# Optimization experiments

Measured on AMD Instinct MI355X. Metric: run time of the kernel, lower is better.

The kernel has to match this reference:

```python
import jax, jax.numpy as jnp
import numpy as np

N_NODES = 100000
N_EDGES = 1600000
N_GRAPHS = 512
HIDDEN = 64
HEADS = 4
HEAD_DIM = HIDDEN // HEADS
IN_FEAT = 32
EDGE_FEAT = 16
N_CLASSES = 10
N_CONV = 3
BN_EPS = 1e-5
BN_BIAS = 1e-4  # torch init: weight=1, bias=0.0001
NEG_SLOPE = 0.2


def batchnorm(x):
    # training-mode BatchNorm1d with weight=1, bias=1e-4 (biased variance, as torch)
    mu = jnp.mean(x, axis=0)
    var = jnp.var(x, axis=0)
    return (x - mu) * jax.lax.rsqrt(var + BN_EPS) + BN_BIAS


def segment_softmax(logits, seg, num_segments):
    # logits: [E] or [E,H]; softmax over edges sharing the same seg id (dst node)
    m = jax.ops.segment_max(logits, seg, num_segments=num_segments)
    e = jnp.exp(logits - m[seg])
    s = jax.ops.segment_sum(e, seg, num_segments=num_segments)
    return e / s[seg]


def setup_inputs() -> dict:
    key = jax.random.key(0)
    ks = jax.random.split(key, 24)
    sd = 0.1
    inp = {}
    inp["x"] = jax.random.normal(ks[0], (N_NODES, IN_FEAT), dtype=jnp.float32)
    inp["edge_attr"] = jax.random.normal(ks[1], (N_EDGES, EDGE_FEAT), dtype=jnp.float32)
    inp["edge_index"] = jax.random.randint(ks[2], (2, N_EDGES), 0, N_NODES)
    inp["batch"] = jnp.sort(jax.random.randint(ks[3], (N_NODES,), 0, N_GRAPHS))
    # EGAT (conv_feat): node/edge linear maps + attention vector
    inp["egat_Wx"] = jax.random.normal(ks[4], (IN_FEAT, HIDDEN), dtype=jnp.float32) * sd
    inp["egat_bx"] = jnp.zeros((HIDDEN,), dtype=jnp.float32)
    inp["egat_We"] = jax.random.normal(ks[5], (EDGE_FEAT, HIDDEN), dtype=jnp.float32) * sd
    inp["egat_be"] = jnp.zeros((HIDDEN,), dtype=jnp.float32)
    inp["egat_att"] = jax.random.normal(ks[6], (HIDDEN,), dtype=jnp.float32) * sd
    # 3 stacked GATConv layers (PyG-style, edge_dim=hidden, concat heads)
    inp["conv_W"] = jax.random.normal(ks[7], (N_CONV, HIDDEN, HIDDEN), dtype=jnp.float32) * sd
    inp["conv_We"] = jax.random.normal(ks[8], (N_CONV, HIDDEN, HIDDEN), dtype=jnp.float32) * sd
    inp["conv_att_src"] = jax.random.normal(ks[9], (N_CONV, HEADS, HEAD_DIM), dtype=jnp.float32) * sd
    inp["conv_att_dst"] = jax.random.normal(ks[10], (N_CONV, HEADS, HEAD_DIM), dtype=jnp.float32) * sd
    inp["conv_att_edge"] = jax.random.normal(ks[11], (N_CONV, HEADS, HEAD_DIM), dtype=jnp.float32) * sd
    inp["conv_bias"] = jnp.zeros((N_CONV, HIDDEN), dtype=jnp.float32)
    # FC head: one hidden Linear (num_fc_layers=2) + classifier
    inp["lin_W"] = jax.random.normal(ks[12], (HIDDEN, HIDDEN), dtype=jnp.float32) * sd
    inp["lin_b"] = jnp.zeros((HIDDEN,), dtype=jnp.float32)
    inp["cls_W"] = jax.random.normal(ks[13], (HIDDEN, N_CLASSES), dtype=jnp.float32) * sd
    inp["cls_b"] = jnp.zeros((N_CLASSES,), dtype=jnp.float32)
    return inp


def reference(x, edge_attr, edge_index, batch,
              egat_Wx, egat_bx, egat_We, egat_be, egat_att,
              conv_W, conv_We, conv_att_src, conv_att_dst, conv_att_edge, conv_bias,
              lin_W, lin_b, cls_W, cls_b):
    src, dst = edge_index[0], edge_index[1]
    n = x.shape[0]

    x = batchnorm(x)

    # EGAT: gather -> attend (leaky_relu + segment softmax over dst) -> scatter-add
    h = x @ egat_Wx + egat_bx            # [N, hidden]
    he = edge_attr @ egat_We + egat_be   # [E, hidden]
    s = jax.nn.leaky_relu((h[src] + h[dst] + he) @ egat_att, NEG_SLOPE)  # [E]
    alpha = segment_softmax(s, dst, n)
    x = jax.ops.segment_sum(alpha[:, None] * h[src], dst, num_segments=n)
    edge = he
    x = jax.nn.relu(x)
    edge = jax.nn.relu(edge)

    # stacked GATConv layers (multi-head, edge features modulate attention)
    for i in range(N_CONV):
        xb = batchnorm(x)
        hh = (xb @ conv_W[i]).reshape(n, HEADS, HEAD_DIM)            # [N,H,D]
        ee = (edge @ conv_We[i]).reshape(-1, HEADS, HEAD_DIM)        # [E,H,D]
        a = (jnp.sum(hh[src] * conv_att_src[i], -1)
             + jnp.sum(hh[dst] * conv_att_dst[i], -1)
             + jnp.sum(ee * conv_att_edge[i], -1))                   # [E,H]
        a = jax.nn.leaky_relu(a, NEG_SLOPE)
        a = segment_softmax(a, dst, n)
        out = jax.ops.segment_sum(a[..., None] * hh[src], dst, num_segments=n)
        x = jax.nn.relu(out.reshape(n, HIDDEN) + conv_bias[i])

    # global add pool over graphs
    x = jax.ops.segment_sum(x, batch, num_segments=N_GRAPHS)  # [G, hidden]

    x = batchnorm(x)
    x = jax.nn.relu(x @ lin_W + lin_b)
    x = batchnorm(x)
    # dropout disabled (eval-mode determinism)
    x = x @ cls_W + cls_b
    return jax.nn.log_softmax(x, axis=-1)
```

## Files before the change

kernel.cpp:

```cpp
#include <hip/hip_runtime.h>
#include <math.h>

#define NN 100000
#define NE 1600000
#define NG 512
#define NCLS 10
#define NEG 0.2f
#define BNEPS 1e-5f
#define BNB 1e-4f
#define MNEG -1e30f

#define NBUK 391
#define CHUNK2 6144
#define NB2 261
#define CAP3 5120

typedef unsigned short u16;
typedef unsigned int u32;
typedef _Float16 f16;
typedef __attribute__((ext_vector_type(8))) f16 f16x8;
typedef __attribute__((ext_vector_type(4))) float f32x4;

__device__ __forceinline__ float lrelu(float v) { return v > 0.f ? v : NEG * v; }
__device__ __forceinline__ u16 f2h(float x) { union { u16 s; f16 h; } c; c.h = (f16)x; return c.s; }
__device__ __forceinline__ float h2f(u16 s) { union { u16 s; f16 h; } c; c.s = s; return (float)c.h; }

template<int C>
__global__ __launch_bounds__(256) void k_bn_part(const float* __restrict__ x, int rows,
                                                 float* __restrict__ part) {
    const int RPI = 256 / C;
    int col = threadIdx.x % C;
    int sub = threadIdx.x / C;
    int nb = gridDim.x;
    int rpb = (rows + nb - 1) / nb;
    int r0 = blockIdx.x * rpb;
    int r1 = min(rows, r0 + rpb);
    float s = 0.f, q = 0.f;
    for (int r = r0 + sub; r < r1; r += RPI) {
        float v = x[(size_t)r * C + col];
        s += v; q += v * v;
    }
    __shared__ float ls[256], lq[256];
    ls[threadIdx.x] = s; lq[threadIdx.x] = q;
    __syncthreads();
    for (int st = RPI / 2; st > 0; st >>= 1) {
        if (sub < st) {
            ls[threadIdx.x] += ls[threadIdx.x + st * C];
            lq[threadIdx.x] += lq[threadIdx.x + st * C];
        }
        __syncthreads();
    }
    if (sub == 0) {
        part[(size_t)blockIdx.x * C + col] = ls[col];
        part[(size_t)(nb + blockIdx.x) * C + col] = lq[col];
    }
}

__global__ __launch_bounds__(256) void k_bn_part16(const u16* __restrict__ x, int rows,
                                                   float* __restrict__ part) {
    int col = threadIdx.x & 63;
    int sub = threadIdx.x >> 6;
    int nb = gridDim.x;
    int rpb = (rows + nb - 1) / nb;
    int r0 = blockIdx.x * rpb;
    int r1 = min(rows, r0 + rpb);
    float s = 0.f, q = 0.f;
    for (int r = r0 + sub; r < r1; r += 4) {
        float v = h2f(x[(size_t)r * 64 + col]);
        s += v; q += v * v;
    }
    __shared__ float ls[256], lq[256];
    ls[threadIdx.x] = s; lq[threadIdx.x] = q;
    __syncthreads();
    for (int st = 2; st > 0; st >>= 1) {
        if (sub < st) {
            ls[threadIdx.x] += ls[threadIdx.x + st * 64];
            lq[threadIdx.x] += lq[threadIdx.x + st * 64];
        }
        __syncthreads();
    }
    if (sub == 0) {
        part[(size_t)blockIdx.x * 64 + col] = ls[col];
        part[(size_t)(nb + blockIdx.x) * 64 + col] = lq[col];
    }
}

__global__ __launch_bounds__(64) void k_bn_adj(const float* __restrict__ part, int nb, int rows, int C,
                                               const float* __restrict__ W, const float* __restrict__ b,
                                               int Ncol, float* __restrict__ sc, float* __restrict__ badj) {
    int c = threadIdx.x;
    __shared__ float shl[64];
    if (c < C) {
        float s = 0.f, q = 0.f;
        for (int bb = 0; bb < nb; bb++) {
            s += part[(size_t)bb * C + c];
            q += part[(size_t)(nb + bb) * C + c];
        }
        float mu = s / rows;
        float var = q / rows - mu * mu;
        float sl = rsqrtf(var + BNEPS);
        sc[c] = sl;
        shl[c] = BNB - mu * sl;
    }
    __syncthreads();
    if (c < Ncol) {
        float a = b ? b[c] : 0.f;
        for (int k = 0; k < C; k++) a += shl[k] * W[(size_t)k * Ncol + c];
        badj[c] = a;
    }
}

template<int C>
__global__ __launch_bounds__(256) void k_bnadjf(const float* __restrict__ part, int nb, int rows,
                                                const float* __restrict__ W, const float* __restrict__ b,
                                                float* __restrict__ badj, u16* __restrict__ Bff) {
    int t = threadIdx.x;
    int c = t & 63, seg = t >> 6;
    __shared__ float rs[4][64], rq[4][64];
    __shared__ float scl[64], shl[64];
    float s = 0.f, q = 0.f;
    if (c < C)
        for (int bb = seg; bb < nb; bb += 4) {
            s += part[(size_t)bb * C + c];
            q += part[(size_t)(nb + bb) * C + c];
        }
    rs[seg][c] = s; rq[seg][c] = q;
    __syncthreads();
    if (t < C) {
        float ss = rs[0][t] + rs[1][t] + rs[2][t] + rs[3][t];
        float qq = rq[0][t] + rq[1][t] + rq[2][t] + rq[3][t];
        float mu = ss / rows;
        float var = qq / rows - mu * mu;
        float sl = rsqrtf(var + BNEPS);
        scl[t] = sl; shl[t] = BNB - mu * sl;
    }
    __syncthreads();
    float a = 0.f;
    for (int k = seg; k < C; k += 4) a += shl[k] * W[(size_t)k * 64 + c];
    rs[seg][c] = a;
    __syncthreads();
    if (t < 64) badj[t] = (b ? b[t] : 0.f) + rs[0][t] + rs[1][t] + rs[2][t] + rs[3][t];
    const int KB = C / 32;
    for (int idx = t; idx < 4 * KB * 64 * 8; idx += 256) {
        int j = idx & 7;
        int lane = (idx >> 3) & 63;
        int kb = (idx >> 9) % KB;
        int ct = idx / (KB * 512);
        int k = kb * 32 + (lane >> 4) * 8 + j;
        int col = ct * 16 + (lane & 15);
        Bff[idx] = f2h(scl[k] * W[(size_t)k * 64 + col]);
    }
}

template<int KB, int EPI, bool F32IN>
__global__ __launch_bounds__(256) void k_gemm_mf(const void* __restrict__ xin,
                                                 const u16* __restrict__ Bff,
                                                 const float* __restrict__ badj,
                                                 u16* __restrict__ outb, int rows,
                                                 const float* __restrict__ att, float* __restrict__ hs,
                                                 const float* __restrict__ as_, const float* __restrict__ ad_,
                                                 float* __restrict__ asrc, float* __restrict__ adst) {
    int wid = threadIdx.x >> 6, lane = threadIdx.x & 63;
    int er = lane & 15, kh = lane >> 4;
    int r0 = blockIdx.x * 64;
    int rw = r0 + wid * 16;
    __shared__ u16 Dl[64][68];
    f16x8 bf[4][KB];
#pragma unroll
    for (int ct = 0; ct < 4; ct++)
#pragma unroll
        for (int kb = 0; kb < KB; kb++)
            bf[ct][kb] = *(const f16x8*)(Bff + ((size_t)(ct * KB + kb) * 64 + lane) * 8);
    f16x8 af[KB];
    int arow = rw + er;
    if (F32IN) {
        const float* xf = (const float*)xin;
        f16x8 av = (f16x8)(f16)0.f;
        if (arow < rows) {
            const float4* p = (const float4*)(xf + (size_t)arow * 32 + kh * 8);
            float4 v0 = p[0], v1 = p[1];
            av[0] = (f16)v0.x; av[1] = (f16)v0.y; av[2] = (f16)v0.z; av[3] = (f16)v0.w;
            av[4] = (f16)v1.x; av[5] = (f16)v1.y; av[6] = (f16)v1.z; av[7] = (f16)v1.w;
        }
        af[0] = av;
    } else {
        const u16* xh = (const u16*)xin;
#pragma unroll
        for (int kb = 0; kb < KB; kb++) {
            f16x8 av = (f16x8)(f16)0.f;
            if (arow < rows) av = *(const f16x8*)(xh + (size_t)arow * 64 + kb * 32 + kh * 8);
            af[kb] = av;
        }
    }
    f32x4 d[4];
#pragma unroll
    for (int ct = 0; ct < 4; ct++) {
        float bj = badj[ct * 16 + er];
        f32x4 cc = {bj, bj, bj, bj};
#pragma unroll
        for (int kb = 0; kb < KB; kb++)
            cc = __builtin_amdgcn_mfma_f32_16x16x32_f16(af[kb], bf[ct][kb], cc, 0, 0, 0);
        d[ct] = cc;
    }
#pragma unroll
    for (int ct = 0; ct < 4; ct++)
#pragma unroll
        for (int r = 0; r < 4; r++)
            Dl[wid * 16 + kh * 4 + r][ct * 16 + er] = f2h(d[ct][r]);
    if (EPI == 1) {
        float av[4];
#pragma unroll
        for (int ct = 0; ct < 4; ct++) av[ct] = att[ct * 16 + er];
#pragma unroll
        for (int r = 0; r < 4; r++) {
            float v = d[0][r] * av[0] + d[1][r] * av[1] + d[2][r] * av[2] + d[3][r] * av[3];
#pragma unroll
            for (int o = 1; o < 16; o <<= 1) v += __shfl_xor(v, o);
            int rr = rw + kh * 4 + r;
            if (er == 0 && rr < rows) hs[rr] = v;
        }
    }
    if (EPI == 2) {
        float a1v[4], a2v[4];
#pragma unroll
        for (int ct = 0; ct < 4; ct++) { a1v[ct] = as_[ct * 16 + er]; a2v[ct] = ad_[ct * 16 + er]; }
#pragma unroll
        for (int ct = 0; ct < 4; ct++) {
#pragma unroll
            for (int r = 0; r < 4; r++) {
                float s1 = d[ct][r] * a1v[ct], s2 = d[ct][r] * a2v[ct];
#pragma unroll
                for (int o = 1; o < 16; o <<= 1) { s1 += __shfl_xor(s1, o); s2 += __shfl_xor(s2, o); }
                int rr = rw + kh * 4 + r;
                if (er == 0 && rr < rows) {
                    asrc[(size_t)rr * 4 + ct] = s1;
                    adst[(size_t)rr * 4 + ct] = s2;
                }
            }
        }
    }
    __syncthreads();
    const u32* D32 = (const u32*)&Dl[0][0];
    u32* out32 = (u32*)outb;
    for (int idx = threadIdx.x; idx < 64 * 32; idx += 256) {
        int r = idx >> 5, c2 = idx & 31;
        int rr = r0 + r;
        if (rr < rows) out32[(size_t)rr * 32 + c2] = D32[r * 34 + c2];
    }
}

__global__ __launch_bounds__(256) void k_gemm_head(const float* __restrict__ x, const float* __restrict__ W,
                                                   const float* __restrict__ sc, const float* __restrict__ badj,
                                                   float* __restrict__ outf, int rows) {
    __shared__ float Ws[64 * 64];
    __shared__ float Xs[32 * 64];
    int r0 = blockIdx.x * 32;
    for (int i = threadIdx.x; i < 64 * 64; i += 256) Ws[i] = W[i];
    for (int i = threadIdx.x; i < 32 * 64; i += 256) {
        int r = i / 64, k = i % 64;
        int rr = r0 + r;
        Xs[i] = (rr < rows) ? x[(size_t)rr * 64 + k] * sc[k] : 0.f;
    }
    __syncthreads();
    int col = threadIdx.x & 63;
    int rg = threadIdx.x >> 6;
    float b0 = badj[col];
    float acc[8];
#pragma unroll
    for (int i = 0; i < 8; i++) acc[i] = b0;
    for (int k = 0; k < 64; k++) {
        float w = Ws[k * 64 + col];
#pragma unroll
        for (int i = 0; i < 8; i++) acc[i] += Xs[(rg * 8 + i) * 64 + k] * w;
    }
#pragma unroll
    for (int i = 0; i < 8; i++) {
        int r = r0 + rg * 8 + i;
        if (r < rows) outf[(size_t)r * 64 + col] = fmaxf(acc[i], 0.f);
    }
}

__global__ __launch_bounds__(768) void k_we(const float* __restrict__ cWe, const float* __restrict__ cae,
                                            const float* __restrict__ Wee, const float* __restrict__ att,
                                            const float* __restrict__ bee, float* __restrict__ wEbuf,
                                            u16* __restrict__ Bf1, u16* __restrict__ Bf2) {
    int t = threadIdx.x;
    int l = t >> 8;
    int h = (t >> 6) & 3;
    int k = t & 63;
    float a = 0.f;
    for (int d = 0; d < 16; d++)
        a += cWe[(size_t)l * 4096 + k * 64 + h * 16 + d] * cae[l * 64 + h * 16 + d];
    wEbuf[t] = a;
    if (t < 16) {
        float v = 0.f;
        for (int j = 0; j < 64; j++) v += Wee[t * 64 + j] * att[j];
        wEbuf[768 + t] = v;
    }
    if (t == 16) {
        float v = 0.f;
        for (int j = 0; j < 64; j++) v += bee[j] * att[j];
        wEbuf[784] = v;
    }
    for (int idx = t; idx < 4 * 64 * 8; idx += 768) {
        int cb = idx >> 9, ln = (idx >> 3) & 63, j = idx & 7;
        int col = cb * 16 + (ln & 15);
        int kk = (ln >> 4) * 8 + j;
        float v = (kk < 16) ? Wee[kk * 64 + col] : 0.f;
        Bf1[idx] = f2h(v);
    }
    __syncthreads();
    for (int idx = t; idx < 2 * 64 * 8; idx += 768) {
        int kb = idx >> 9, ln = (idx >> 3) & 63, j = idx & 7;
        int n = ln & 15;
        int kk = kb * 32 + (ln >> 4) * 8 + j;
        float v = (n < 12) ? wEbuf[n * 64 + kk] : 0.f;
        Bf2[idx] = f2h(v);
    }
}

__global__ __launch_bounds__(256) void k_bhist(const int* __restrict__ dst, int* __restrict__ hist) {
    __shared__ int lh[512];
    int t = threadIdx.x;
    lh[t] = 0; lh[t + 256] = 0;
    __syncthreads();
    int base = blockIdx.x * CHUNK2;
    int cnt = min(CHUNK2, NE - base);
    for (int i = t; i < cnt; i += 256) atomicAdd(&lh[dst[base + i] >> 8], 1);
    __syncthreads();
    for (int b = t; b < NBUK; b += 256) hist[blockIdx.x * NBUK + b] = lh[b];
}

__global__ __launch_bounds__(256) void k_colsum(const int* __restrict__ hist, int* __restrict__ colsum) {
    int col = blockIdx.x;
    int t = threadIdx.x;
    int s = 0;
    for (int b = t; b < NB2; b += 256) s += hist[b * NBUK + col];
    __shared__ int ls[256];
    ls[t] = s;
    __syncthreads();
    for (int st = 128; st; st >>= 1) {
        if (t < st) ls[t] += ls[t + st];
        __syncthreads();
    }
    if (t == 0) colsum[col] = ls[0];
}

__global__ __launch_bounds__(512) void k_bukscan(const int* __restrict__ colsum,
                                                 int* __restrict__ bucketBase, int* __restrict__ rowp) {
    __shared__ int ls[512];
    int t = threadIdx.x;
    int v = (t < NBUK) ? colsum[t] : 0;
    ls[t] = v;
    __syncthreads();
    for (int off = 1; off < 512; off <<= 1) {
        int a = (t >= off) ? ls[t - off] : 0;
        __syncthreads();
        ls[t] += a;
        __syncthreads();
    }
    if (t < NBUK) bucketBase[t] = ls[t] - v;
    if (t == 0) { bucketBase[NBUK] = NE; rowp[NN] = NE; }
}

__global__ __launch_bounds__(512) void k_coloffs(const int* __restrict__ hist,
                                                 const int* __restrict__ bucketBase, int* __restrict__ offs) {
    int col = blockIdx.x;
    int t = threadIdx.x;
    __shared__ int ls[512];
    int v = (t < NB2) ? hist[(size_t)t * NBUK + col] : 0;
    ls[t] = v;
    __syncthreads();
    for (int off = 1; off < 512; off <<= 1) {
        int a = (t >= off) ? ls[t - off] : 0;
        __syncthreads();
        ls[t] += a;
        __syncthreads();
    }
    if (t < NB2) offs[(size_t)t * NBUK + col] = bucketBase[col] + ls[t] - v;
}

__global__ __launch_bounds__(256) void k_part(const int* __restrict__ src, const int* __restrict__ dst,
                                              const int* __restrict__ offs, int2* __restrict__ seTmp) {
    __shared__ int lhist[512];
    __shared__ int lstart[NBUK + 1];
    __shared__ int lcur[NBUK];
    __shared__ int loffs[NBUK];
    __shared__ int2 stage[CHUNK2];
    int t = threadIdx.x;
    int base = blockIdx.x * CHUNK2;
    int cnt = min(CHUNK2, NE - base);
    int blkrow = blockIdx.x * NBUK;
    lhist[t] = 0; lhist[t + 256] = 0;
    __syncthreads();
    for (int i = t; i < cnt; i += 256) atomicAdd(&lhist[dst[base + i] >> 8], 1);
    __syncthreads();
    for (int off = 1; off < 512; off <<= 1) {
        int v0 = (t >= off) ? lhist[t - off] : 0;
        int v1 = lhist[t + 256 - off];
        __syncthreads();
        lhist[t] += v0; lhist[t + 256] += v1;
        __syncthreads();
    }
    if (t == 0) lstart[0] = 0;
    lstart[t + 1] = lhist[t];
    if (t + 257 <= NBUK) lstart[t + 257] = lhist[t + 256];
    __syncthreads();
    for (int b = t; b < NBUK; b += 256) {
        lcur[b] = lstart[b];
        loffs[b] = offs[blkrow + b];
    }
    __syncthreads();
    for (int i = t; i < cnt; i += 256) {
        int e = base + i;
        int d = dst[e];
        int b = d >> 8;
        int pos = atomicAdd(&lcur[b], 1);
        int2 v; v.x = src[e] | (b << 17); v.y = e | ((d & 255) << 21);
        stage[pos] = v;
    }
    __syncthreads();
    for (int q = t; q < cnt; q += 256) {
        int2 v = stage[q];
        int b = ((u32)v.x) >> 17;
        int2 o; o.x = v.x & 0x1FFFF; o.y = v.y;
        seTmp[loffs[b] + (q - lstart[b])] = o;
    }
}

__global__ __launch_bounds__(256) void k_bucket(const int2* __restrict__ seTmp,
                                                const int* __restrict__ bucketBase,
                                                int2* __restrict__ se, int* __restrict__ rowp) {
    int b = blockIdx.x;
    int t = threadIdx.x;
    int beg = bucketBase[b], end = bucketBase[b + 1];
    int cnt = end - beg;
    __shared__ int lhist[256], lscan[256], lcur[256];
    __shared__ int2 ebuf[CAP3];
    lhist[t] = 0;
    __syncthreads();
    for (int i = t; i < cnt; i += 256)
        atomicAdd(&lhist[((u32)seTmp[beg + i].y) >> 21], 1);
    __syncthreads();
    lscan[t] = lhist[t];
    __syncthreads();
    for (int off = 1; off < 256; off <<= 1) {
        int v = (t >= off) ? lscan[t - off] : 0;
        __syncthreads();
        lscan[t] += v;
        __syncthreads();
    }
    int excl = lscan[t] - lhist[t];
    lcur[t] = excl;
    int node = b * 256 + t;
    if (node < NN) rowp[node] = beg + excl;
    __syncthreads();
    if (cnt <= CAP3) {
        for (int i = t; i < cnt; i += 256) {
            int2 v = seTmp[beg + i];
            int dl = ((u32)v.y) >> 21;
            int pos = atomicAdd(&lcur[dl], 1);
            int2 o; o.x = v.x; o.y = v.y & 0x1FFFFF;
            ebuf[pos] = o;
        }
        __syncthreads();
        for (int q = t; q < cnt; q += 256) se[beg + q] = ebuf[q];
    } else {
        for (int i = t; i < cnt; i += 256) {
            int2 v = seTmp[beg + i];
            int dl = ((u32)v.y) >> 21;
            int pos = atomicAdd(&lcur[dl], 1);
            int2 o; o.x = v.x; o.y = v.y & 0x1FFFFF;
            se[beg + pos] = o;
        }
    }
}

__global__ __launch_bounds__(256) void k_edgepre(const float* __restrict__ ea,
                                                 const u16* __restrict__ Bf1, const u16* __restrict__ Bf2,
                                                 const float* __restrict__ bee, const float* __restrict__ wEbuf,
                                                 const int2* __restrict__ se,
                                                 float* __restrict__ heatt, ushort4* __restrict__ aedH) {
    int wid = threadIdx.x >> 6, lane = threadIdx.x & 63;
    int gw = blockIdx.x * 4 + wid;
    int p0 = gw * 16;
    __shared__ f16 Pl[4][16][72];
    __shared__ f16 D2l[4][16][20];
    f16x8 bf1[4], bf2[2];
#pragma unroll
    for (int cb = 0; cb < 4; cb++) bf1[cb] = *(const f16x8*)(Bf1 + ((size_t)cb * 64 + lane) * 8);
#pragma unroll
    for (int kb = 0; kb < 2; kb++) bf2[kb] = *(const f16x8*)(Bf2 + ((size_t)kb * 64 + lane) * 8);
    int er = lane & 15, kh = lane >> 4;
    f16x8 af = (f16x8)(f16)0.f;
    float part = 0.f;
    if (kh < 2) {
        int e = se[p0 + er].y;
        const float4* pa = (const float4*)(ea + (size_t)e * 16 + kh * 8);
        float4 v0 = pa[0], v1 = pa[1];
        af[0] = (f16)v0.x; af[1] = (f16)v0.y; af[2] = (f16)v0.z; af[3] = (f16)v0.w;
        af[4] = (f16)v1.x; af[5] = (f16)v1.y; af[6] = (f16)v1.z; af[7] = (f16)v1.w;
        const float* va = wEbuf + 768 + kh * 8;
        part = v0.x * va[0] + v0.y * va[1] + v0.z * va[2] + v0.w * va[3]
             + v1.x * va[4] + v1.y * va[5] + v1.z * va[6] + v1.w * va[7];
    }
    float po = __shfl_xor(part, 16);
    if (lane < 16) heatt[p0 + lane] = part + po + wEbuf[784];
    f32x4 z = {0.f, 0.f, 0.f, 0.f};
    f32x4 d0 = __builtin_amdgcn_mfma_f32_16x16x32_f16(af, bf1[0], z, 0, 0, 0);
    f32x4 d1 = __builtin_amdgcn_mfma_f32_16x16x32_f16(af, bf1[1], z, 0, 0, 0);
    f32x4 d2_ = __builtin_amdgcn_mfma_f32_16x16x32_f16(af, bf1[2], z, 0, 0, 0);
    f32x4 d3 = __builtin_amdgcn_mfma_f32_16x16x32_f16(af, bf1[3], z, 0, 0, 0);
    {
        float b0 = bee[0 * 16 + er], b1 = bee[1 * 16 + er], b2 = bee[2 * 16 + er], b3 = bee[3 * 16 + er];
#pragma unroll
        for (int r = 0; r < 4; r++) {
            int row = kh * 4 + r;
            Pl[wid][row][0 * 16 + er] = (f16)fmaxf(d0[r] + b0, 0.f);
            Pl[wid][row][1 * 16 + er] = (f16)fmaxf(d1[r] + b1, 0.f);
            Pl[wid][row][2 * 16 + er] = (f16)fmaxf(d2_[r] + b2, 0.f);
            Pl[wid][row][3 * 16 + er] = (f16)fmaxf(d3[r] + b3, 0.f);
        }
    }
    __syncthreads();
    f16x8 pa0 = *(const f16x8*)&Pl[wid][er][kh * 8];
    f16x8 pa1 = *(const f16x8*)&Pl[wid][er][32 + kh * 8];
    f32x4 dd = __builtin_amdgcn_mfma_f32_16x16x32_f16(pa0, bf2[0], z, 0, 0, 0);
    dd = __builtin_amdgcn_mfma_f32_16x16x32_f16(pa1, bf2[1], dd, 0, 0, 0);
#pragma unroll
    for (int r = 0; r < 4; r++) D2l[wid][kh * 4 + r][er] = (f16)dd[r];
    __syncthreads();
    int e2 = lane & 15, l3 = lane >> 4;
    if (l3 < 3) {
        ushort4 o = *(const ushort4*)&D2l[wid][e2][l3 * 4];
        aedH[(size_t)l3 * NE + p0 + e2] = o;
    }
}

__global__ __launch_bounds__(256) void k_egat_agg(const int* __restrict__ rowp, const int2* __restrict__ se,
                                                  const float* __restrict__ heatt, const float* __restrict__ hs,
                                                  const u16* __restrict__ hb, u16* __restrict__ xout) {
    int wid = threadIdx.x >> 6, lane = threadIdx.x & 63;
    int n = blockIdx.x * 4 + wid;
    if (n >= NN) return;
    int beg = rowp[n], deg = rowp[n + 1] - beg;
    if (deg == 0) { xout[(size_t)n * 64 + lane] = 0; return; }
    float hsn = hs[n];
    int half = lane >> 5;
    int c0 = (lane & 31) * 2;
    if (deg <= 64) {
        int s = 0; float lg = MNEG;
        if (lane < deg) {
            int2 pr = se[beg + lane];
            s = pr.x;
            lg = lrelu(hs[s] + hsn + heatt[beg + lane]);
        }
        float m = lg;
#pragma unroll
        for (int o = 32; o; o >>= 1) m = fmaxf(m, __shfl_xor(m, o));
        float e = (lane < deg) ? __expf(lg - m) : 0.f;
        float sm = e;
#pragma unroll
        for (int o = 32; o; o >>= 1) sm += __shfl_xor(sm, o);
        float p = e * (1.f / sm);
        float a0 = 0.f, a1 = 0.f, a2 = 0.f, a3 = 0.f;
        for (int j = 0; j < deg; j += 4) {
            int j0 = j + half, j1 = j + 2 + half;
            int s0 = __shfl(s, j0); float p0 = __shfl(p, j0);
            int s1 = __shfl(s, j1); float p1 = __shfl(p, j1);
            u32 v0 = *(const u32*)(hb + (size_t)s0 * 64 + c0);
            u32 v1 = *(const u32*)(hb + (size_t)s1 * 64 + c0);
            a0 = fmaf(p0, h2f((u16)v0), a0);
            a1 = fmaf(p0, h2f((u16)(v0 >> 16)), a1);
            a2 = fmaf(p1, h2f((u16)v1), a2);
            a3 = fmaf(p1, h2f((u16)(v1 >> 16)), a3);
        }
        a0 += a2; a1 += a3;
        a0 += __shfl_xor(a0, 32);
        a1 += __shfl_xor(a1, 32);
        if (lane < 32) {
            u32 o = (u32)f2h(fmaxf(a0, 0.f)) | ((u32)f2h(fmaxf(a1, 0.f)) << 16);
            ((u32*)xout)[(size_t)n * 32 + (lane & 31)] = o;
        }
    } else {
        float m = MNEG, sm = 0.f;
        for (int i = lane; i < deg; i += 64) {
            int2 pr = se[beg + i];
            float v = lrelu(hs[pr.x] + hsn + heatt[beg + i]);
            float mn = fmaxf(m, v);
            sm = sm * __expf(m - mn) + __expf(v - mn);
            m = mn;
        }
#pragma unroll
        for (int o = 32; o; o >>= 1) {
            float mo = __shfl_xor(m, o), so = __shfl_xor(sm, o);
            float mn = fmaxf(m, mo);
            sm = sm * __expf(m - mn) + so * __expf(mo - mn);
            m = mn;
        }
        float inv = 1.f / sm;
        float acc0 = 0.f;
        for (int base = 0; base < deg; base += 64) {
            int i = base + lane;
            int s = 0; float p = 0.f;
            if (i < deg) {
                int2 pr = se[beg + i];
                s = pr.x;
                p = __expf(lrelu(hs[s] + hsn + heatt[beg + i]) - m) * inv;
            }
            int mm = min(64, deg - base);
            for (int j = 0; j < mm; j++) {
                int s0 = __shfl(s, j); float q0 = __shfl(p, j);
                acc0 = fmaf(q0, h2f(hb[(size_t)s0 * 64 + lane]), acc0);
            }
        }
        xout[(size_t)n * 64 + lane] = f2h(fmaxf(acc0, 0.f));
    }
}

__global__ __launch_bounds__(256) void k_conv_agg(const int* __restrict__ rowp, const int2* __restrict__ se,
                                                  const ushort4* __restrict__ aedH, const float* __restrict__ asrc,
                                                  const float* __restrict__ adst, const u16* __restrict__ hb,
                                                  const float* __restrict__ bias, u16* __restrict__ xout) {
    int wid = threadIdx.x >> 6, lane = threadIdx.x & 63;
    int n = blockIdx.x * 4 + wid;
    if (n >= NN) return;
    int beg = rowp[n], deg = rowp[n + 1] - beg;
    if (deg == 0) { xout[(size_t)n * 64 + lane] = f2h(fmaxf(bias[lane], 0.f)); return; }
    float4 an = ((const float4*)adst)[n];
    __shared__ float pls[4][4][72];
    __shared__ int sl[4][64];
    int half = lane >> 5;
    int c0 = (lane & 31) * 2;
    if (deg <= 64) {
        int s = 0;
        float l0 = MNEG, l1 = MNEG, l2 = MNEG, l3 = MNEG;
        if (lane < deg) {
            s = se[beg + lane].x;
            float4 as4 = ((const float4*)asrc)[s];
            ushort4 u = aedH[beg + lane];
            l0 = lrelu(as4.x + an.x + h2f(u.x));
            l1 = lrelu(as4.y + an.y + h2f(u.y));
            l2 = lrelu(as4.z + an.z + h2f(u.z));
            l3 = lrelu(as4.w + an.w + h2f(u.w));
        }
        float m0 = l0, m1 = l1, m2 = l2, m3 = l3;
#pragma unroll
        for (int o = 32; o; o >>= 1) {
            m0 = fmaxf(m0, __shfl_xor(m0, o)); m1 = fmaxf(m1, __shfl_xor(m1, o));
            m2 = fmaxf(m2, __shfl_xor(m2, o)); m3 = fmaxf(m3, __shfl_xor(m3, o));
        }
        float e0 = (lane < deg) ? __expf(l0 - m0) : 0.f;
        float e1 = (lane < deg) ? __expf(l1 - m1) : 0.f;
        float e2 = (lane < deg) ? __expf(l2 - m2) : 0.f;
        float e3 = (lane < deg) ? __expf(l3 - m3) : 0.f;
        float s0 = e0, s1 = e1, s2 = e2, s3 = e3;
#pragma unroll
        for (int o = 32; o; o >>= 1) {
            s0 += __shfl_xor(s0, o); s1 += __shfl_xor(s1, o);
            s2 += __shfl_xor(s2, o); s3 += __shfl_xor(s3, o);
        }
        pls[wid][0][lane] = e0 * (1.f / s0);
        pls[wid][1][lane] = e1 * (1.f / s1);
        pls[wid][2][lane] = e2 * (1.f / s2);
        pls[wid][3][lane] = e3 * (1.f / s3);
        sl[wid][lane] = s;
        __builtin_amdgcn_wave_barrier();
        int head = (lane & 31) >> 3;
        const float* prow = &pls[wid][head][0];
        const int* srow = &sl[wid][0];
        float a0 = 0.f, a1 = 0.f, a2 = 0.f, a3 = 0.f;
        for (int j = 0; j < deg; j += 4) {
            int j0 = j + half, j1 = j + 2 + half;
            float p0 = prow[j0]; int sj0 = srow[j0];
            float p1 = prow[j1]; int sj1 = srow[j1];
            u32 v0 = *(const u32*)(hb + (size_t)sj0 * 64 + c0);
            u32 v1 = *(const u32*)(hb + (size_t)sj1 * 64 + c0);
            a0 = fmaf(p0, h2f((u16)v0), a0);
            a1 = fmaf(p0, h2f((u16)(v0 >> 16)), a1);
            a2 = fmaf(p1, h2f((u16)v1), a2);
            a3 = fmaf(p1, h2f((u16)(v1 >> 16)), a3);
        }
        a0 += a2; a1 += a3;
        a0 += __shfl_xor(a0, 32);
        a1 += __shfl_xor(a1, 32);
        if (lane < 32) {
            u32 o = (u32)f2h(fmaxf(a0 + bias[c0], 0.f)) | ((u32)f2h(fmaxf(a1 + bias[c0 + 1], 0.f)) << 16);
            ((u32*)xout)[(size_t)n * 32 + (lane & 31)] = o;
        }
    } else {
        int hq = lane >> 4;
        float m0 = MNEG, m1 = MNEG, m2 = MNEG, m3 = MNEG;
        float s0 = 0.f, s1 = 0.f, s2 = 0.f, s3 = 0.f;
        for (int i = lane; i < deg; i += 64) {
            int s = se[beg + i].x;
            float4 as4 = ((const float4*)asrc)[s];
            ushort4 u = aedH[beg + i];
            float l0 = lrelu(as4.x + an.x + h2f(u.x));
            float l1 = lrelu(as4.y + an.y + h2f(u.y));
            float l2 = lrelu(as4.z + an.z + h2f(u.z));
            float l3 = lrelu(as4.w + an.w + h2f(u.w));
            float n0 = fmaxf(m0, l0); s0 = s0 * __expf(m0 - n0) + __expf(l0 - n0); m0 = n0;
            float n1 = fmaxf(m1, l1); s1 = s1 * __expf(m1 - n1) + __expf(l1 - n1); m1 = n1;
            float n2 = fmaxf(m2, l2); s2 = s2 * __expf(m2 - n2) + __expf(l2 - n2); m2 = n2;
            float n3 = fmaxf(m3, l3); s3 = s3 * __expf(m3 - n3) + __expf(l3 - n3); m3 = n3;
        }
#pragma unroll
        for (int o = 32; o; o >>= 1) {
            float mo, so, mn;
            mo = __shfl_xor(m0, o); so = __shfl_xor(s0, o); mn = fmaxf(m0, mo);
            s0 = s0 * __expf(m0 - mn) + so * __expf(mo - mn); m0 = mn;
            mo = __shfl_xor(m1, o); so = __shfl_xor(s1, o); mn = fmaxf(m1, mo);
            s1 = s1 * __expf(m1 - mn) + so * __expf(mo - mn); m1 = mn;
            mo = __shfl_xor(m2, o); so = __shfl_xor(s2, o); mn = fmaxf(m2, mo);
            s2 = s2 * __expf(m2 - mn) + so * __expf(mo - mn); m2 = mn;
            mo = __shfl_xor(m3, o); so = __shfl_xor(s3, o); mn = fmaxf(m3, mo);
            s3 = s3 * __expf(m3 - mn) + so * __expf(mo - mn); m3 = mn;
        }
        float i0 = 1.f / s0, i1 = 1.f / s1, i2 = 1.f / s2, i3 = 1.f / s3;
        float acc0 = 0.f;
        for (int base = 0; base < deg; base += 64) {
            int i = base + lane;
            if (i < deg) {
                int s = se[beg + i].x;
                float4 as4 = ((const float4*)asrc)[s];
                ushort4 u = aedH[beg + i];
                pls[wid][0][lane] = __expf(lrelu(as4.x + an.x + h2f(u.x)) - m0) * i0;
                pls[wid][1][lane] = __expf(lrelu(as4.y + an.y + h2f(u.y)) - m1) * i1;
                pls[wid][2][lane] = __expf(lrelu(as4.z + an.z + h2f(u.z)) - m2) * i2;
                pls[wid][3][lane] = __expf(lrelu(as4.w + an.w + h2f(u.w)) - m3) * i3;
                sl[wid][lane] = s;
            }
            __builtin_amdgcn_wave_barrier();
            int mm = min(64, deg - base);
            const float* prow = &pls[wid][hq][0];
            const int* srow = &sl[wid][0];
            for (int j = 0; j < mm; j++)
                acc0 = fmaf(prow[j], h2f(hb[(size_t)srow[j] * 64 + lane]), acc0);
            __builtin_amdgcn_wave_barrier();
        }
        xout[(size_t)n * 64 + lane] = f2h(fmaxf(acc0 + bias[lane], 0.f));
    }
}

__device__ __forceinline__ int lowerb(const int* a, int n, int key) {
    int lo = 0, hi = n;
    while (lo < hi) {
        int mid = (lo + hi) >> 1;
        if (a[mid] < key) lo = mid + 1; else hi = mid;
    }
    return lo;
}

__global__ __launch_bounds__(256) void k_pool(const u16* __restrict__ x, const int* __restrict__ batch,
                                              float* __restrict__ g) {
    int gr = blockIdx.x;
    int lane = threadIdx.x & 63;
    int sub = threadIdx.x >> 6;
    int beg = lowerb(batch, NN, gr);
    int end = lowerb(batch, NN, gr + 1);
    float acc = 0.f;
    for (int i = beg + sub; i < end; i += 4) acc += h2f(x[(size_t)i * 64 + lane]);
    __shared__ float ls[4][64];
    ls[sub][lane] = acc;
    __syncthreads();
    if (sub == 0)
        g[(size_t)gr * 64 + lane] = ls[0][lane] + ls[1][lane] + ls[2][lane] + ls[3][lane];
}

__global__ __launch_bounds__(64) void k_cls(const float* __restrict__ y, const float* __restrict__ W,
                                            const float* __restrict__ sc, const float* __restrict__ badj,
                                            float* __restrict__ out) {
    int r = blockIdx.x, lane = threadIdx.x;
    __shared__ float yr[64];
    yr[lane] = y[(size_t)r * 64 + lane] * sc[lane];
    __syncthreads();
    float lg = -INFINITY;
    if (lane < NCLS) {
        float a = badj[lane];
        for (int k = 0; k < 64; k++) a += yr[k] * W[k * NCLS + lane];
        lg = a;
    }
    float mx = lg;
#pragma unroll
    for (int o = 32; o; o >>= 1) mx = fmaxf(mx, __shfl_xor(mx, o));
    float e = (lane < NCLS) ? expf(lg - mx) : 0.f;
    float s = e;
#pragma unroll
    for (int o = 32; o; o >>= 1) s += __shfl_xor(s, o);
    if (lane < NCLS) out[(size_t)r * NCLS + lane] = lg - mx - logf(s);
}

extern "C" void kernel_launch(void* const* d_in, const int* in_sizes, int n_in,
                              void* d_out, int out_size, void* d_ws, size_t ws_size,
                              hipStream_t stream) {
    const float* x0  = (const float*)d_in[0];
    const float* ea  = (const float*)d_in[1];
    const int* eidx  = (const int*)d_in[2];
    const int* batch = (const int*)d_in[3];
    const float* Wx  = (const float*)d_in[4];
    const float* bx  = (const float*)d_in[5];
    const float* Wee = (const float*)d_in[6];
    const float* bee = (const float*)d_in[7];
    const float* att = (const float*)d_in[8];
    const float* cW  = (const float*)d_in[9];
    const float* cWe = (const float*)d_in[10];
    const float* cas = (const float*)d_in[11];
    const float* cad = (const float*)d_in[12];
    const float* cae = (const float*)d_in[13];
    const float* cb  = (const float*)d_in[14];
    const float* lW  = (const float*)d_in[15];
    const float* lb  = (const float*)d_in[16];
    const float* clW = (const float*)d_in[17];
    const float* clb = (const float*)d_in[18];
    float* out = (float*)d_out;

    const int* srcA = eidx;
    const int* dstA = eidx + NE;

    char* w = (char*)d_ws;
    size_t off = 0;
    auto alloc = [&](size_t bytes) -> void* {
        void* p = w + off;
        off += (bytes + 255) & ~(size_t)255;
        return p;
    };
    u16* hbA      = (u16*)alloc((size_t)NN * 64 * 2);
    u16* B16      = (u16*)alloc((size_t)NN * 64 * 2);
    float* hs     = (float*)alloc((size_t)NN * 4);
    float* asrc   = (float*)alloc((size_t)NN * 4 * 4);
    float* adst   = (float*)alloc((size_t)NN * 4 * 4);
    float* heatt  = (float*)alloc((size_t)NE * 4);
    ushort4* aedH = (ushort4*)alloc((size_t)3 * NE * 8);
    int2* se      = (int2*)alloc((size_t)NE * 8);
    int* rowp     = (int*)alloc((size_t)(NN + 1) * 4);
    int* hist     = (int*)alloc((size_t)NB2 * NBUK * 4);
    int* offs     = (int*)alloc((size_t)NB2 * NBUK * 4);
    int* bucketBase = (int*)alloc((size_t)(NBUK + 1) * 4);
    int* colsum   = (int*)alloc((size_t)NBUK * 4);
    float* part   = (float*)alloc((size_t)2 * 200 * 64 * 4);
    float* badj   = (float*)alloc(64 * 4);
    float* wEbuf  = (float*)alloc(800 * 4);
    u16* Bf1      = (u16*)alloc(4 * 64 * 8 * 2);
    u16* Bf2      = (u16*)alloc(2 * 64 * 8 * 2);
    u16* Bff      = (u16*)alloc(8 * 64 * 8 * 2);
    float* g      = (float*)alloc((size_t)NG * 64 * 4);
    float* y      = (float*)alloc((size_t)NG * 64 * 4);
    float* badj2  = (float*)alloc(64 * 4);
    float* badj3  = (float*)alloc(64 * 4);
    float* sc2    = (float*)alloc(64 * 4);
    float* sc3    = (float*)alloc(64 * 4);
    if (off > ws_size) return;

    int2* seTmp = (int2*)aedH;

    const int NB = 200;
    const int GEMMB = (NN + 63) / 64;

    k_bhist<<<NB2, 256, 0, stream>>>(dstA, hist);
    k_colsum<<<NBUK, 256, 0, stream>>>(hist, colsum);
    k_bukscan<<<1, 512, 0, stream>>>(colsum, bucketBase, rowp);
    k_coloffs<<<NBUK, 512, 0, stream>>>(hist, bucketBase, offs);
    k_part<<<NB2, 256, 0, stream>>>(srcA, dstA, offs, seTmp);
    k_bucket<<<NBUK, 256, 0, stream>>>(seTmp, bucketBase, se, rowp);

    k_we<<<1, 768, 0, stream>>>(cWe, cae, Wee, att, bee, wEbuf, Bf1, Bf2);

    k_bn_part<32><<<NB, 256, 0, stream>>>(x0, NN, part);
    k_bnadjf<32><<<1, 256, 0, stream>>>(part, NB, NN, Wx, bx, badj, Bff);
    k_gemm_mf<1, 1, true><<<GEMMB, 256, 0, stream>>>(
        x0, Bff, badj, hbA, NN, att, hs, nullptr, nullptr, nullptr, nullptr);

    k_edgepre<<<NE / 64, 256, 0, stream>>>(ea, Bf1, Bf2, bee, wEbuf, se, heatt, aedH);

    k_egat_agg<<<(NN + 3) / 4, 256, 0, stream>>>(rowp, se, heatt, hs, hbA, B16);

    for (int l = 0; l < 3; l++) {
        k_bn_part16<<<NB, 256, 0, stream>>>(B16, NN, part);
        k_bnadjf<64><<<1, 256, 0, stream>>>(part, NB, NN, cW + (size_t)l * 4096, nullptr, badj, Bff);
        k_gemm_mf<2, 2, false><<<GEMMB, 256, 0, stream>>>(
            B16, Bff, badj, hbA, NN, nullptr, nullptr,
            cas + l * 64, cad + l * 64, asrc, adst);
        k_conv_agg<<<(NN + 3) / 4, 256, 0, stream>>>(rowp, se, aedH + (size_t)l * NE, asrc, adst, hbA,
                                                     cb + l * 64, B16);
    }

    k_pool<<<NG, 256, 0, stream>>>(B16, batch, g);

    k_bn_part<64><<<2, 256, 0, stream>>>(g, NG, part);
    k_bn_adj<<<1, 64, 0, stream>>>(part, 2, NG, 64, lW, lb, 64, sc2, badj2);
    k_gemm_head<<<(NG + 31) / 32, 256, 0, stream>>>(g, lW, sc2, badj2, y, NG);

    k_bn_part<64><<<2, 256, 0, stream>>>(y, NG, part);
    k_bn_adj<<<1, 64, 0, stream>>>(part, 2, NG, 64, clW, clb, 10, sc3, badj3);
    k_cls<<<NG, 64, 0, stream>>>(y, clW, sc3, badj3, out);
}
```

Baseline: 707.9 us.

## Process 32 edges per wave in edgepre and unroll aggregation gathers by 8

The edge precompute kernel now handles 32 edges per wave instead of 16. All 64 lanes load edge attributes into shared memory, and block-wide __syncthreads is replaced by wave barriers, which halves the grid and amortizes the weight-fragment loads. The EGAT and conv aggregation loops are unrolled to issue four independent neighbor gathers per iteration with more accumulators, giving more memory-level parallelism. Costs are higher register and LDS use, and relying on wave barriers assumes the shared-memory accesses stay within one wave. The unrolled loop reads up to 8 past deg, which relies on padding or masked probabilities being zero.

```diff
diff --git a/kernel.cpp b/kernel.cpp
--- a/kernel.cpp
+++ b/kernel.cpp
@@ -482,58 +482,80 @@
                                                  const int2* __restrict__ se,
                                                  float* __restrict__ heatt, ushort4* __restrict__ aedH) {
     int wid = threadIdx.x >> 6, lane = threadIdx.x & 63;
-    int gw = blockIdx.x * 4 + wid;
-    int p0 = gw * 16;
-    __shared__ f16 Pl[4][16][72];
-    __shared__ f16 D2l[4][16][20];
+    int p0 = (blockIdx.x * 4 + wid) * 32;
+    __shared__ f16 EaD[4][32][24];
+    __shared__ f16 Pl[4][32][72];
     f16x8 bf1[4], bf2[2];
 #pragma unroll
     for (int cb = 0; cb < 4; cb++) bf1[cb] = *(const f16x8*)(Bf1 + ((size_t)cb * 64 + lane) * 8);
 #pragma unroll
     for (int kb = 0; kb < 2; kb++) bf2[kb] = *(const f16x8*)(Bf2 + ((size_t)kb * 64 + lane) * 8);
+    int e = lane & 31, q = lane >> 5;
+    int ei = se[p0 + e].y;
+    const float4* pa = (const float4*)(ea + (size_t)ei * 16 + q * 8);
+    float4 v0 = pa[0], v1 = pa[1];
+    {
+        const float* va = wEbuf + 768 + q * 8;
+        float part = v0.x * va[0] + v0.y * va[1] + v0.z * va[2] + v0.w * va[3]
+                   + v1.x * va[4] + v1.y * va[5] + v1.z * va[6] + v1.w * va[7];
+        float po = __shfl_xor(part, 32);
+        if (lane < 32) heatt[p0 + e] = part + po + wEbuf[784];
+    }
+    {
+        f16x8 t;
+        t[0] = (f16)v0.x; t[1] = (f16)v0.y; t[2] = (f16)v0.z; t[3] = (f16)v0.w;
+        t[4] = (f16)v1.x; t[5] = (f16)v1.y; t[6] = (f16)v1.z; t[7] = (f16)v1.w;
+        *(f16x8*)&EaD[wid][e][q * 8] = t;
+    }
+    __builtin_amdgcn_wave_barrier();
     int er = lane & 15, kh = lane >> 4;
-    f16x8 af = (f16x8)(f16)0.f;
-    float part = 0.f;
+    f16x8 a0f = (f16x8)(f16)0.f, a1f = (f16x8)(f16)0.f;
     if (kh < 2) {
-        int e = se[p0 + er].y;
-        const float4* pa = (const float4*)(ea + (size_t)e * 16 + kh * 8);
-        float4 v0 = pa[0], v1 = pa[1];
-        af[0] = (f16)v0.x; af[1] = (f16)v0.y; af[2] = (f16)v0.z; af[3] = (f16)v0.w;
-        af[4] = (f16)v1.x; af[5] = (f16)v1.y; af[6] = (f16)v1.z; af[7] = (f16)v1.w;
-        const float* va = wEbuf + 768 + kh * 8;
-        part = v0.x * va[0] + v0.y * va[1] + v0.z * va[2] + v0.w * va[3]
-             + v1.x * va[4] + v1.y * va[5] + v1.z * va[6] + v1.w * va[7];
-    }
-    float po = __shfl_xor(part, 16);
-    if (lane < 16) heatt[p0 + lane] = part + po + wEbuf[784];
+        a0f = *(const f16x8*)&EaD[wid][er][kh * 8];
+        a1f = *(const f16x8*)&EaD[wid][16 + er][kh * 8];
+    }
     f32x4 z = {0.f, 0.f, 0.f, 0.f};
-    f32x4 d0 = __builtin_amdgcn_mfma_f32_16x16x32_f16(af, bf1[0], z, 0, 0, 0);
-    f32x4 d1 = __builtin_amdgcn_mfma_f32_16x16x32_f16(af, bf1[1], z, 0, 0, 0);
-    f32x4 d2_ = __builtin_amdgcn_mfma_f32_16x16x32_f16(af, bf1[2], z, 0, 0, 0);
-    f32x4 d3 = __builtin_amdgcn_mfma_f32_16x16x32_f16(af, bf1[3], z, 0, 0, 0);
+    f32x4 d0[4], d1[4];
+#pragma unroll
+    for (int ct = 0; ct < 4; ct++) {
+        d0[ct] = __builtin_amdgcn_mfma_f32_16x16x32_f16(a0f, bf1[ct], z, 0, 0, 0);
+        d1[ct] = __builtin_amdgcn_mfma_f32_16x16x32_f16(a1f, bf1[ct], z, 0, 0, 0);
+    }
     {
-        float b0 = bee[0 * 16 + er], b1 = bee[1 * 16 + er], b2 = bee[2 * 16 + er], b3 = bee[3 * 16 + er];
-#pragma unroll
-        for (int r = 0; r < 4; r++) {
-            int row = kh * 4 + r;
-            Pl[wid][row][0 * 16 + er] = (f16)fmaxf(d0[r] + b0, 0.f);
-            Pl[wid][row][1 * 16 + er] = (f16)fmaxf(d1[r] + b1, 0.f);
-            Pl[wid][row][2 * 16 + er] = (f16)fmaxf(d2_[r] + b2, 0.f);
-            Pl[wid][row][3 * 16 + er] = (f16)fmaxf(d3[r] + b3, 0.f);
-        }
-    }
-    __syncthreads();
-    f16x8 pa0 = *(const f16x8*)&Pl[wid][er][kh * 8];
-    f16x8 pa1 = *(const f16x8*)&Pl[wid][er][32 + kh * 8];
-    f32x4 dd = __builtin_amdgcn_mfma_f32_16x16x32_f16(pa0, bf2[0], z, 0, 0, 0);
-    dd = __builtin_amdgcn_mfma_f32_16x16x32_f16(pa1, bf2[1], dd, 0, 0, 0);
-#pragma unroll
-    for (int r = 0; r < 4; r++) D2l[wid][kh * 4 + r][er] = (f16)dd[r];
-    __syncthreads();
-    int e2 = lane & 15, l3 = lane >> 4;
-    if (l3 < 3) {
-        ushort4 o = *(const ushort4*)&D2l[wid][e2][l3 * 4];
+#pragma unroll
+        for (int ct = 0; ct < 4; ct++) {
+            float bb = bee[ct * 16 + er];
+#pragma unroll
+            for (int r = 0; r < 4; r++) {
+                Pl[wid][kh * 4 + r][ct * 16 + er] = (f16)fmaxf(d0[ct][r] + bb, 0.f);
+                Pl[wid][16 + kh * 4 + r][ct * 16 + er] = (f16)fmaxf(d1[ct][r] + bb, 0.f);
+            }
+        }
+    }
+    __builtin_amdgcn_wave_barrier();
+    f16x8 pa00 = *(const f16x8*)&Pl[wid][er][kh * 8];
+    f16x8 pa01 = *(const f16x8*)&Pl[wid][er][32 + kh * 8];
+    f16x8 pa10 = *(const f16x8*)&Pl[wid][16 + er][kh * 8];
+    f16x8 pa11 = *(const f16x8*)&Pl[wid][16 + er][32 + kh * 8];
+    f32x4 dd0 = __builtin_amdgcn_mfma_f32_16x16x32_f16(pa00, bf2[0], z, 0, 0, 0);
+    dd0 = __builtin_amdgcn_mfma_f32_16x16x32_f16(pa01, bf2[1], dd0, 0, 0, 0);
+    f32x4 dd1 = __builtin_amdgcn_mfma_f32_16x16x32_f16(pa10, bf2[0], z, 0, 0, 0);
+    dd1 = __builtin_amdgcn_mfma_f32_16x16x32_f16(pa11, bf2[1], dd1, 0, 0, 0);
+    __builtin_amdgcn_wave_barrier();
+#pragma unroll
+    for (int r = 0; r < 4; r++) {
+        EaD[wid][kh * 4 + r][er] = (f16)dd0[r];
+        EaD[wid][16 + kh * 4 + r][er] = (f16)dd1[r];
+    }
+    __builtin_amdgcn_wave_barrier();
+    {
+        int e2 = lane & 31, l3 = lane >> 5;
+        ushort4 o = *(const ushort4*)&EaD[wid][e2][l3 * 4];
         aedH[(size_t)l3 * NE + p0 + e2] = o;
+        if (lane < 32) {
+            ushort4 o2 = *(const ushort4*)&EaD[wid][lane][8];
+            aedH[(size_t)2 * NE + p0 + lane] = o2;
+        }
     }
 }
 
@@ -564,18 +586,26 @@
         for (int o = 32; o; o >>= 1) sm += __shfl_xor(sm, o);
         float p = e * (1.f / sm);
         float a0 = 0.f, a1 = 0.f, a2 = 0.f, a3 = 0.f;
-        for (int j = 0; j < deg; j += 4) {
-            int j0 = j + half, j1 = j + 2 + half;
-            int s0 = __shfl(s, j0); float p0 = __shfl(p, j0);
-            int s1 = __shfl(s, j1); float p1 = __shfl(p, j1);
+        float a4 = 0.f, a5 = 0.f, a6 = 0.f, a7 = 0.f;
+        for (int j = 0; j < deg; j += 8) {
+            int j0 = j + half, j1 = j + 2 + half, j2 = j + 4 + half, j3 = j + 6 + half;
+            int s0 = __shfl(s, j0), s1 = __shfl(s, j1), s2 = __shfl(s, j2), s3 = __shfl(s, j3);
+            float p0 = __shfl(p, j0), p1 = __shfl(p, j1), p2 = __shfl(p, j2), p3 = __shfl(p, j3);
             u32 v0 = *(const u32*)(hb + (size_t)s0 * 64 + c0);
             u32 v1 = *(const u32*)(hb + (size_t)s1 * 64 + c0);
+            u32 v2 = *(const u32*)(hb + (size_t)s2 * 64 + c0);
+            u32 v3 = *(const u32*)(hb + (size_t)s3 * 64 + c0);
             a0 = fmaf(p0, h2f((u16)v0), a0);
             a1 = fmaf(p0, h2f((u16)(v0 >> 16)), a1);
             a2 = fmaf(p1, h2f((u16)v1), a2);
             a3 = fmaf(p1, h2f((u16)(v1 >> 16)), a3);
-        }
-        a0 += a2; a1 += a3;
+            a4 = fmaf(p2, h2f((u16)v2), a4);
+            a5 = fmaf(p2, h2f((u16)(v2 >> 16)), a5);
+            a6 = fmaf(p3, h2f((u16)v3), a6);
+            a7 = fmaf(p3, h2f((u16)(v3 >> 16)), a7);
+        }
+        a0 += a2 + a4 + a6;
+        a1 += a3 + a5 + a7;
         a0 += __shfl_xor(a0, 32);
         a1 += __shfl_xor(a1, 32);
         if (lane < 32) {
@@ -670,18 +700,28 @@
         const float* prow = &pls[wid][head][0];
         const int* srow = &sl[wid][0];
         float a0 = 0.f, a1 = 0.f, a2 = 0.f, a3 = 0.f;
-        for (int j = 0; j < deg; j += 4) {
-            int j0 = j + half, j1 = j + 2 + half;
+        float a4 = 0.f, a5 = 0.f, a6 = 0.f, a7 = 0.f;
+        for (int j = 0; j < deg; j += 8) {
+            int j0 = j + half, j1 = j + 2 + half, j2 = j + 4 + half, j3 = j + 6 + half;
             float p0 = prow[j0]; int sj0 = srow[j0];
             float p1 = prow[j1]; int sj1 = srow[j1];
+            float p2 = prow[j2]; int sj2 = srow[j2];
+            float p3 = prow[j3]; int sj3 = srow[j3];
             u32 v0 = *(const u32*)(hb + (size_t)sj0 * 64 + c0);
             u32 v1 = *(const u32*)(hb + (size_t)sj1 * 64 + c0);
+            u32 v2 = *(const u32*)(hb + (size_t)sj2 * 64 + c0);
+            u32 v3 = *(const u32*)(hb + (size_t)sj3 * 64 + c0);
             a0 = fmaf(p0, h2f((u16)v0), a0);
             a1 = fmaf(p0, h2f((u16)(v0 >> 16)), a1);
             a2 = fmaf(p1, h2f((u16)v1), a2);
             a3 = fmaf(p1, h2f((u16)(v1 >> 16)), a3);
-        }
-        a0 += a2; a1 += a3;
+            a4 = fmaf(p2, h2f((u16)v2), a4);
+            a5 = fmaf(p2, h2f((u16)(v2 >> 16)), a5);
+            a6 = fmaf(p3, h2f((u16)v3), a6);
+            a7 = fmaf(p3, h2f((u16)(v3 >> 16)), a7);
+        }
+        a0 += a2 + a4 + a6;
+        a1 += a3 + a5 + a7;
         a0 += __shfl_xor(a0, 32);
         a1 += __shfl_xor(a1, 32);
         if (lane < 32) {
@@ -871,7 +911,7 @@
     k_gemm_mf<1, 1, true><<<GEMMB, 256, 0, stream>>>(
         x0, Bff, badj, hbA, NN, att, hs, nullptr, nullptr, nullptr, nullptr);
 
-    k_edgepre<<<NE / 64, 256, 0, stream>>>(ea, Bf1, Bf2, bee, wEbuf, se, heatt, aedH);
+    k_edgepre<<<NE / 128, 256, 0, stream>>>(ea, Bf1, Bf2, bee, wEbuf, se, heatt, aedH);
 
     k_egat_agg<<<(NN + 3) / 4, 256, 0, stream>>>(rowp, se, heatt, hs, hbA, B16);
 
```

Result: faster. 691.3 us (-2.3%).
